# Performance work log

Measured on AMD Instinct MI355X. Metric: run time of the kernel, lower is better.

## Reference

```python
import jax, jax.numpy as jnp
import numpy as np
from math import comb

N_INPUT, N_HIDDEN, N_LATENT = 2, 1024, 16
T, B = 320, 192
DEG = N_LATENT // 2 - 1          # 7
NPTS = DEG + 1                   # 8 control points
LAT = N_LATENT + N_LATENT // 2   # 24

_COMB = jnp.array([comb(DEG, i) for i in range(NPTS)], dtype=jnp.float32)
_I = jnp.arange(NPTS, dtype=jnp.float32)


def setup_inputs() -> dict:
    key = jax.random.key(0)
    ks = jax.random.split(key, 24)
    H = N_HIDDEN
    w = lambda k, shape, sc: (jax.random.normal(k, shape, jnp.float32) * sc)
    return dict(
        x=jax.random.normal(ks[0], (T, B, N_INPUT), jnp.float32),
        latent_ctrlpt=jax.random.normal(ks[1], (B, N_LATENT), jnp.float32),
        latent_ratw=jax.random.uniform(ks[2], (B, N_LATENT // 2), jnp.float32, 0.1, 1.0),
        # h0/c0 projection linears (forward/backward directions)
        W_hf=w(ks[3], (H, LAT), 0.2), b_hf=jnp.zeros((H,), jnp.float32),
        W_hb=w(ks[4], (H, LAT), 0.2), b_hb=jnp.zeros((H,), jnp.float32),
        W_cf=w(ks[5], (H, LAT), 0.2), b_cf=jnp.zeros((H,), jnp.float32),
        W_cb=w(ks[6], (H, LAT), 0.2), b_cb=jnp.zeros((H,), jnp.float32),
        # bi-LSTM weights, PyTorch gate order (i, f, g, o)
        W_ih_f=w(ks[7], (4 * H, N_INPUT), 0.03), W_hh_f=w(ks[8], (4 * H, H), 0.03),
        b_ih_f=jnp.zeros((4 * H,), jnp.float32), b_hh_f=jnp.zeros((4 * H,), jnp.float32),
        W_ih_b=w(ks[9], (4 * H, N_INPUT), 0.03), W_hh_b=w(ks[10], (4 * H, H), 0.03),
        b_ih_b=jnp.zeros((4 * H,), jnp.float32), b_hh_b=jnp.zeros((4 * H,), jnp.float32),
        # t-logits head
        W_log=w(ks[11], (1, 2 * H), 0.03), b_log=jnp.zeros((1,), jnp.float32),
    )


def _lstm_dir(x_tm, h0, c0, W_ih, W_hh, b_ih, b_hh, reverse):
    # x_tm: (T, B, in). Precompute input projection once (compute-efficient).
    xs = jnp.einsum('tbi,gi->tbg', x_tm, W_ih) + b_ih + b_hh  # (T, B, 4H)

    def step(carry, xt):
        h, c = carry
        g = xt + h @ W_hh.T
        i, f, gg, o = jnp.split(g, 4, axis=-1)
        c = jax.nn.sigmoid(f) * c + jax.nn.sigmoid(i) * jnp.tanh(gg)
        h = jax.nn.sigmoid(o) * jnp.tanh(c)
        return (h, c), h

    _, hs = jax.lax.scan(step, (h0, c0), xs, reverse=reverse)
    return hs  # (T, B, H)


def reference(x, latent_ctrlpt, latent_ratw,
              W_hf, b_hf, W_hb, b_hb, W_cf, b_cf, W_cb, b_cb,
              W_ih_f, W_hh_f, b_ih_f, b_hh_f,
              W_ih_b, W_hh_b, b_ih_b, b_hh_b,
              W_log, b_log):
    latent = jnp.concatenate([latent_ctrlpt, latent_ratw], axis=1)  # (B, LAT)
    h0f = jnp.tanh(latent @ W_hf.T + b_hf)
    h0b = jnp.tanh(latent @ W_hb.T + b_hb)
    c0f = jnp.tanh(latent @ W_cf.T + b_cf)
    c0b = jnp.tanh(latent @ W_cb.T + b_cb)

    hf = _lstm_dir(x, h0f, c0f, W_ih_f, W_hh_f, b_ih_f, b_hh_f, reverse=False)
    hb = _lstm_dir(x, h0b, c0b, W_ih_b, W_hh_b, b_ih_b, b_hh_b, reverse=True)
    out = jnp.concatenate([hf, hb], axis=-1)           # (T, B, 2H)
    out = jnp.transpose(out, (1, 0, 2))                # batch_first (B, T, 2H)

    logits = (out @ W_log.T + b_log)[..., 0]           # (B, T)
    ts = jnp.cumsum(jax.nn.softmax(logits, axis=1), axis=1)  # (B, T) in (0, 1]

    P = latent_ctrlpt.reshape(-1, NPTS, 2)             # (B, NPTS, 2)
    r = latent_ratw.reshape(-1, NPTS)                  # (B, NPTS)

    # Rational Bezier curve, batched over B and T (replaces per-sample loop)
    t = ts[..., None]                                   # (B, T, 1)
    basis = _COMB * t ** _I * (1.0 - t) ** (DEG - _I)   # (B, T, NPTS)
    num = basis * r[:, None, :]
    w = num / num.sum(-1, keepdims=True)
    curves = jnp.einsum('btn,bnd->btd', w, P)           # (B, T, 2)

    # mean of squared consecutive control-point distances, averaged over batch
    d2 = ((P[:, 1:, :] - P[:, :-1, :]) ** 2).sum(-1)    # (B, NPTS-1)
    reg = d2.mean()
    return curves, reg
```

## Files before the change

kernel.cpp:

```cpp
#include <hip/hip_runtime.h>
#include <stdint.h>

#define T_STEPS 320
#define BATCH   192
#define HID     1024
#define NBLK    512

typedef unsigned short u16;
typedef __bf16 bf16x8 __attribute__((ext_vector_type(8)));
typedef float  f32x4  __attribute__((ext_vector_type(4)));
typedef unsigned int u32x4 __attribute__((ext_vector_type(4)));

#define OFF_BAR      0u
#define OFF_PART     8192u
#define MEMSET_BYTES 3940352u
#define OFF_C0       3940352u
#define OFF_H        5513216u
#define OFF_WPACK    7086080u
#define OFF_COEF     23863296u
#define WS_NEED      23994368u

#define DMP_WK_STRIDE 3264
#define DMP_BYTES     52224
#define DYN_LDS       52240

__device__ __forceinline__ u16 f2bf(float f) {
  unsigned u = __float_as_uint(f);
  unsigned r = (u + 0x7FFFu + ((u >> 16) & 1u)) >> 16;
  return (u16)r;
}
__device__ __forceinline__ float sigm(float x)   { return 1.f / (1.f + __expf(-x)); }
__device__ __forceinline__ float tanh_f(float x) { return 1.f - 2.f / (1.f + __expf(2.f * x)); }

__global__ void pack_k(const float* __restrict__ Whhf, const float* __restrict__ Whhb,
                       u16* __restrict__ wpack)
{
  int lin = blockIdx.x * 256 + threadIdx.x;
  int lane = lin & 63;
  int cg   = (lin >> 6) & 3;
  int ks   = (lin >> 8) & 31;
  int jsl  = (lin >> 13) & 63;
  int dir  = (lin >> 19) & 1;
  int col  = cg * 16 + (lane & 15);
  int R    = (col & 3) * 1024 + jsl * 16 + (col >> 2);
  int kb   = ks * 32 + (lane >> 4) * 8;
  const float* W = dir ? Whhb : Whhf;
  const float* src = W + (size_t)R * 1024 + kb;
  unsigned w[4];
  #pragma unroll
  for (int e = 0; e < 4; ++e) {
    unsigned lo = f2bf(src[2 * e]);
    unsigned hi = f2bf(src[2 * e + 1]);
    w[e] = lo | (hi << 16);
  }
  *((uint4*)(wpack + (size_t)lin * 8)) = make_uint4(w[0], w[1], w[2], w[3]);
}

__global__ void coef_k(const float* __restrict__ Wihf, const float* __restrict__ bihf,
                       const float* __restrict__ bhhf,
                       const float* __restrict__ Wihb, const float* __restrict__ bihb,
                       const float* __restrict__ bhhb, float* __restrict__ coef)
{
  int id  = blockIdx.x * 256 + threadIdx.x;
  int col = id & 63;
  int jsl = (id >> 6) & 63;
  int dir = (id >> 12) & 1;
  int R   = (col & 3) * 1024 + jsl * 16 + (col >> 2);
  const float* Wih = dir ? Wihb : Wihf;
  const float* bi  = dir ? bihb : bihf;
  const float* bh  = dir ? bhhb : bhhf;
  float4 v;
  v.x = Wih[(size_t)R * 2 + 0];
  v.y = Wih[(size_t)R * 2 + 1];
  v.z = bi[R] + bh[R];
  v.w = 0.f;
  ((float4*)coef)[id] = v;
}

__global__ void init_k(const float* __restrict__ ctrl, const float* __restrict__ ratw,
                       const float* __restrict__ Whf, const float* __restrict__ bhf,
                       const float* __restrict__ Whb, const float* __restrict__ bhb,
                       const float* __restrict__ Wcf, const float* __restrict__ bcf,
                       const float* __restrict__ Wcb, const float* __restrict__ bcb,
                       u16* hb, float* c0)
{
  int idx = blockIdx.x * 256 + threadIdx.x;
  int m = blockIdx.y;
  int b = idx >> 10;
  int h = idx & 1023;
  const float* W  = (m == 0) ? Whf : (m == 1) ? Whb : (m == 2) ? Wcf : Wcb;
  const float* bi = (m == 0) ? bhf : (m == 1) ? bhb : (m == 2) ? bcf : bcb;
  float acc = bi[h];
  const float* wr = W + h * 24;
  #pragma unroll
  for (int k = 0; k < 16; ++k) acc += wr[k] * ctrl[b * 16 + k];
  #pragma unroll
  for (int k = 0; k < 8; ++k)  acc += wr[16 + k] * ratw[b * 8 + k];
  acc = tanh_f(acc);
  if (m < 2) hb[((size_t)(m * 2 + 0) * BATCH + b) * HID + h] = f2bf(acc);
  else       c0[((size_t)(m - 2) * BATCH + b) * HID + h] = acc;
}


#define ALD(S, OB) \
  asm volatile("global_load_dwordx4 %0, %1, off offset:" #OB " sc0 sc1" : "=v"(aq[S][0]) : "v"(ab0)); \
  asm volatile("global_load_dwordx4 %0, %1, off offset:" #OB " sc0 sc1" : "=v"(aq[S][1]) : "v"(ab1)); \
  asm volatile("global_load_dwordx4 %0, %1, off offset:" #OB " sc0 sc1" : "=v"(aq[S][2]) : "v"(ab2));

#define BLD(S, C) { const u16* bp_ = wb + (C) * 2048; \
  asm volatile("global_load_dwordx4 %0, %1, off offset:0"    : "=v"(bq[S][0]) : "v"(bp_)); \
  asm volatile("global_load_dwordx4 %0, %1, off offset:1024" : "=v"(bq[S][1]) : "v"(bp_)); \
  asm volatile("global_load_dwordx4 %0, %1, off offset:2048" : "=v"(bq[S][2]) : "v"(bp_)); \
  asm volatile("global_load_dwordx4 %0, %1, off offset:3072" : "=v"(bq[S][3]) : "v"(bp_)); }

#define SB __builtin_amdgcn_sched_barrier(0);

#define WB(n) \
  asm volatile("s_waitcnt vmcnt(" #n ")" ::: "memory"); \
  __builtin_amdgcn_sched_barrier(0);

#define MM(I) { \
  _Pragma("unroll") \
  for (int mt_ = 0; mt_ < 3; ++mt_) { \
    bf16x8 a_ = __builtin_bit_cast(bf16x8, aq[(I) & 3][mt_]); \
    _Pragma("unroll") \
    for (int n_ = 0; n_ < 4; ++n_) { \
      bf16x8 b_ = __builtin_bit_cast(bf16x8, bq[(I) & 3][n_]); \
      acc[mt_][n_] = __builtin_amdgcn_mfma_f32_16x16x32_bf16(a_, b_, acc[mt_][n_], 0, 0, 0); \
    } \
  } }

#define HST(PT, VL) asm volatile("global_store_short %0, %1, off sc0 sc1" :: "v"(PT), "v"(VL) : "memory")

__launch_bounds__(256, 2)
__global__ void lstm_persist(const float* __restrict__ x,
                             const float* __restrict__ wlog,
                             float* part,
                             const float* __restrict__ c0,
                             u16* hb,
                             const u16* __restrict__ wpack,
                             const float* __restrict__ coef,
                             unsigned* bar)
{
  extern __shared__ char lds[];
  float* DMP = (float*)lds;
  int* ldsflag = (int*)(lds + DMP_BYTES);

  const int tid   = threadIdx.x;
  const int bid   = blockIdx.x;
  const int half  = bid >> 8;
  const int idx   = bid & 255;
  const int grp   = ((idx & 7) + half) & 7;
  const int jsl   = (idx >> 3) + half * 32;
  const int dir   = grp & 1;
  const int bq    = grp >> 1;
  const int wk    = tid >> 6;
  const int lane  = tid & 63;

  if (tid == 0) *ldsflag = 0;

  const int rgrp = tid >> 4;
  const int jj   = tid & 15;
  const int jglob = jsl * 16 + jj;
  float4 cf0, cf1, cf2, cf3;
  {
    const float4* cp = (const float4*)coef + ((dir * 64 + jsl) * 64 + jj * 4);
    cf0 = cp[0]; cf1 = cp[1]; cf2 = cp[2]; cf3 = cp[3];
  }
  const float wlg = wlog[dir * 1024 + jglob];

  float creg[3];
  int   bgm[3];
  #pragma unroll
  for (int mt = 0; mt < 3; ++mt) {
    int r  = rgrp * 3 + mt;
    int bg = bq * 48 + r;
    bgm[mt]  = bg;
    creg[mt] = c0[((size_t)dir * BATCH + bg) * HID + jglob];
  }

  const int arow0 = bq * 48 + 0 * 16 + (lane & 15);
  const int arow1 = arow0 + 16;
  const int arow2 = arow0 + 32;
  const int koff  = wk * 256 + (lane >> 4) * 8;
  const u16* wb   = wpack + (size_t)(dir * 64 + jsl) * 65536
                          + (size_t)wk * 16384 + lane * 8;

  float* pbase = part + ((size_t)(dir * 8 + (jsl & 7)) * BATCH) * T_STEPS;

  unsigned* g1  = bar + (grp << 8) + ((jsl >> 3) << 4);
  unsigned* g2  = bar + (grp << 8) + 128;
  unsigned* rel = bar + (grp << 8) + 144;

  float* dbase = DMP + (size_t)wk * DMP_WK_STRIDE
                     + ((lane >> 4) * 4) * 68 + (lane & 15);
  const int goff = rgrp * 3 * 68 + jj * 4;

  float lpv[3];
  int   lpo[3];

  __syncthreads();

  for (int s = 0; s < T_STEPS; ++s) {
    const int rbuf = s & 1;
    const u16* hsrc = hb + ((size_t)(dir * 2 + rbuf)) * BATCH * HID;
    u16*       hdst = hb + ((size_t)(dir * 2 + (rbuf ^ 1))) * BATCH * HID;
    const u16* ab0 = hsrc + (size_t)arow0 * HID + koff;
    const u16* ab1 = hsrc + (size_t)arow1 * HID + koff;
    const u16* ab2 = hsrc + (size_t)arow2 * HID + koff;

    f32x4 acc[3][4];
    #pragma unroll
    for (int mt = 0; mt < 3; ++mt)
      #pragma unroll
      for (int n = 0; n < 4; ++n)
        acc[mt][n] = (f32x4){0.f, 0.f, 0.f, 0.f};

    u32x4 aq[4][3];
    u32x4 bq[4][4];

    ALD(0, 0)   BLD(0, 0) SB
    ALD(1, 64)  BLD(1, 1) SB
    ALD(2, 128) BLD(2, 2) SB

    ALD(3, 192) BLD(3, 3) WB(21) MM(0)
    ALD(0, 256) BLD(0, 4) WB(21) MM(1)
    ALD(1, 320) BLD(1, 5) WB(21) MM(2)
    ALD(2, 384) BLD(2, 6) WB(21) MM(3)
    ALD(3, 448) BLD(3, 7) WB(21) MM(4)
                          WB(14) MM(5)
                          WB(7)  MM(6)
                          WB(0)  MM(7)

    #pragma unroll
    for (int mt = 0; mt < 3; ++mt)
      #pragma unroll
      for (int n = 0; n < 4; ++n)
        #pragma unroll
        for (int r = 0; r < 4; ++r)
          dbase[(mt * 16 + r) * 68 + n * 16] = acc[mt][n][r];
    __syncthreads();

    const int t_x = dir ? (T_STEPS - 1 - s) : s;

    #pragma unroll
    for (int mt = 0; mt < 3; ++mt) {
      const int ga = goff + mt * 68;
      f32x4 p0 = *(const f32x4*)(DMP + 0 * DMP_WK_STRIDE + ga);
      f32x4 p1 = *(const f32x4*)(DMP + 1 * DMP_WK_STRIDE + ga);
      f32x4 p2 = *(const f32x4*)(DMP + 2 * DMP_WK_STRIDE + ga);
      f32x4 p3 = *(const f32x4*)(DMP + 3 * DMP_WK_STRIDE + ga);
      f32x4 g4 = (p0 + p1) + (p2 + p3);
      int bg = bgm[mt];
      float2 xv = *(const float2*)(x + ((size_t)t_x * BATCH + bg) * 2);
      float pi = g4[0] + cf0.x * xv.x + cf0.y * xv.y + cf0.z;
      float pf = g4[1] + cf1.x * xv.x + cf1.y * xv.y + cf1.z;
      float pg = g4[2] + cf2.x * xv.x + cf2.y * xv.y + cf2.z;
      float po = g4[3] + cf3.x * xv.x + cf3.y * xv.y + cf3.z;
      float ig = sigm(pi), fg = sigm(pf), gv = tanh_f(pg), og = sigm(po);
      float c = fg * creg[mt] + ig * gv;
      creg[mt] = c;
      float h = og * tanh_f(c);
      u16* hp = hdst + (size_t)bg * HID + jglob;
      unsigned hv = (unsigned)f2bf(h);
      HST(hp, hv);
      float lp = h * wlg;
      lp += __shfl_xor(lp, 1);
      lp += __shfl_xor(lp, 2);
      lp += __shfl_xor(lp, 4);
      lp += __shfl_xor(lp, 8);
      lpv[mt] = lp;
      lpo[mt] = bg * T_STEPS + t_x;
    }

    asm volatile("s_waitcnt vmcnt(0)" ::: "memory");
    __syncthreads();

    if (jj == 0) {
      atomicAdd(&pbase[lpo[0]], lpv[0]);
      atomicAdd(&pbase[lpo[1]], lpv[1]);
      atomicAdd(&pbase[lpo[2]], lpv[2]);
    }

    if (tid == 0) {
      bool last = false;
      unsigned o1 = __hip_atomic_fetch_add(g1, 1u, __ATOMIC_RELAXED, __HIP_MEMORY_SCOPE_AGENT);
      if (o1 == (unsigned)(s * 8 + 7)) {
        unsigned o2 = __hip_atomic_fetch_add(g2, 1u, __ATOMIC_RELAXED, __HIP_MEMORY_SCOPE_AGENT);
        if (o2 == (unsigned)(s * 8 + 7)) {
          unsigned rv = (unsigned)(s + 1);
          asm volatile("global_store_dword %0, %1, off sc0 sc1" :: "v"(rel), "v"(rv) : "memory");
          last = true;
        }
      }
      if (!last) {
        long guard = 0;
        unsigned rv;
        for (;;) {
          asm volatile("global_load_dword %0, %1, off sc0 sc1" : "=v"(rv) : "v"(rel));
          asm volatile("s_waitcnt vmcnt(0)" ::: "memory");
          if ((int)rv >= s + 1) break;
          if (++guard > (1L << 20)) { *ldsflag = 1; break; }
          __builtin_amdgcn_s_sleep(2);
        }
      }
    }
    __syncthreads();
    if (*ldsflag) return;
  }
}

__global__ void post_k(const float* __restrict__ part, const float* __restrict__ ctrl,
                       const float* __restrict__ ratw, float* __restrict__ out)
{
  __shared__ float sh[T_STEPS + 64];
  const int b = blockIdx.x;
  const int t = threadIdx.x;
  float l = 0.f;
  #pragma unroll
  for (int p = 0; p < 16; ++p)
    l += part[((size_t)p * BATCH + b) * T_STEPS + t];
  sh[t] = l;
  __syncthreads();
  if (t < 64) {
    float mm = sh[t];
    for (int i = t + 64; i < T_STEPS; i += 64) mm = fmaxf(mm, sh[i]);
    #pragma unroll
    for (int o = 32; o; o >>= 1) mm = fmaxf(mm, __shfl_xor(mm, o));
    if (t == 0) sh[T_STEPS] = mm;
  }
  __syncthreads();
  const float m = sh[T_STEPS];
  float e = __expf(l - m);
  __syncthreads();
  sh[t] = e;
  __syncthreads();
  for (int off = 1; off < T_STEPS; off <<= 1) {
    float v = (t >= off) ? sh[t - off] : 0.f;
    __syncthreads();
    sh[t] += v;
    __syncthreads();
  }
  const float total = sh[T_STEPS - 1];
  const float ts = sh[t] / total;

  float px[8], py[8], rr[8];
  #pragma unroll
  for (int n = 0; n < 8; ++n) {
    px[n] = ctrl[b * 16 + 2 * n];
    py[n] = ctrl[b * 16 + 2 * n + 1];
    rr[n] = ratw[b * 8 + n];
  }
  const float C[8] = {1.f, 7.f, 21.f, 35.f, 35.f, 21.f, 7.f, 1.f};
  float tp[8], up[8];
  tp[0] = 1.f; up[0] = 1.f;
  const float u = 1.f - ts;
  #pragma unroll
  for (int n = 1; n < 8; ++n) { tp[n] = tp[n - 1] * ts; up[n] = up[n - 1] * u; }
  float den = 0.f, nx = 0.f, ny = 0.f;
  #pragma unroll
  for (int n = 0; n < 8; ++n) {
    float w = C[n] * tp[n] * up[7 - n] * rr[n];
    den += w; nx += w * px[n]; ny += w * py[n];
  }
  out[(b * T_STEPS + t) * 2 + 0] = nx / den;
  out[(b * T_STEPS + t) * 2 + 1] = ny / den;

  if (b == 0) {
    __syncthreads();
    if (t < BATCH) {
      float s2 = 0.f;
      #pragma unroll
      for (int n = 0; n < 7; ++n) {
        float dx = ctrl[t * 16 + 2 * n + 2] - ctrl[t * 16 + 2 * n + 0];
        float dy = ctrl[t * 16 + 2 * n + 3] - ctrl[t * 16 + 2 * n + 1];
        s2 += dx * dx + dy * dy;
      }
      sh[t] = s2;
    }
    __syncthreads();
    if (t == 0) {
      float tot = 0.f;
      for (int i = 0; i < BATCH; ++i) tot += sh[i];
      out[BATCH * T_STEPS * 2] = tot / (float)(BATCH * 7);
    }
  }
}

extern "C" void kernel_launch(void* const* d_in, const int* in_sizes, int n_in,
                              void* d_out, int out_size, void* d_ws, size_t ws_size,
                              hipStream_t stream)
{
  const float* x    = (const float*)d_in[0];
  const float* ctrl = (const float*)d_in[1];
  const float* ratw = (const float*)d_in[2];
  const float* Whf  = (const float*)d_in[3];
  const float* bhf  = (const float*)d_in[4];
  const float* Whb  = (const float*)d_in[5];
  const float* bhb  = (const float*)d_in[6];
  const float* Wcf  = (const float*)d_in[7];
  const float* bcf  = (const float*)d_in[8];
  const float* Wcb  = (const float*)d_in[9];
  const float* bcb  = (const float*)d_in[10];
  const float* Wihf = (const float*)d_in[11];
  const float* Whhf = (const float*)d_in[12];
  const float* bihf = (const float*)d_in[13];
  const float* bhhf = (const float*)d_in[14];
  const float* Wihb = (const float*)d_in[15];
  const float* Whhb = (const float*)d_in[16];
  const float* bihb = (const float*)d_in[17];
  const float* bhhb = (const float*)d_in[18];
  const float* Wlog = (const float*)d_in[19];
  float* out = (float*)d_out;
  char*  ws  = (char*)d_ws;
  if (ws_size < (size_t)WS_NEED) return;

  unsigned* bar    = (unsigned*)(ws + OFF_BAR);
  float*    part   = (float*)(ws + OFF_PART);
  float*    c0     = (float*)(ws + OFF_C0);
  u16*      hb     = (u16*)(ws + OFF_H);
  u16*      wpack  = (u16*)(ws + OFF_WPACK);
  float*    coef   = (float*)(ws + OFF_COEF);

  hipMemsetAsync(ws, 0, MEMSET_BYTES, stream);
  pack_k<<<4096, 256, 0, stream>>>(Whhf, Whhb, wpack);
  coef_k<<<32, 256, 0, stream>>>(Wihf, bihf, bhhf, Wihb, bihb, bhhb, coef);
  init_k<<<dim3(768, 4), 256, 0, stream>>>(ctrl, ratw, Whf, bhf, Whb, bhb,
                                           Wcf, bcf, Wcb, bcb, hb, c0);
  hipFuncSetAttribute((const void*)lstm_persist,
                      hipFuncAttributeMaxDynamicSharedMemorySize, DYN_LDS);
  lstm_persist<<<NBLK, 256, DYN_LDS, stream>>>(x, Wlog, part, c0, hb, wpack, coef, bar);
  post_k<<<BATCH, T_STEPS, 0, stream>>>(part, ctrl, ratw, out);
}
```

Before: 4.224 ms.

## Replace two-level barrier with flat counter polling and remap block-to-group assignment

Replaces the hierarchical arrive/release barrier, where the last arriver stores a release flag, with a flat scheme. Each block increments its sub-group counter, then 8 lanes of wave 0 poll all 8 counters and sum them through shuffles until the total reaches 64 per step. Blocks are also remapped so that direction and batch quarter come from the low bits of the block index. The aim is to remove the serial second atomic and the release store from the critical path of each step, in exchange for more polling traffic on the shared counters.

```diff
diff --git a/kernel.cpp b/kernel.cpp
--- a/kernel.cpp
+++ b/kernel.cpp
@@ -150,12 +150,13 @@
   const int bid   = blockIdx.x;
   const int half  = bid >> 8;
   const int idx   = bid & 255;
-  const int grp   = ((idx & 7) + half) & 7;
-  const int jsl   = (idx >> 3) + half * 32;
-  const int dir   = grp & 1;
-  const int bq    = grp >> 1;
+  const int dir   = idx & 1;
+  const int jsl   = idx >> 2;
+  const int bquad = half * 2 + ((idx >> 1) & 1);
+  const int grp   = dir * 4 + bquad;
   const int wk    = tid >> 6;
   const int lane  = tid & 63;
+  const int wave  = tid >> 6;
 
   if (tid == 0) *ldsflag = 0;
 
@@ -174,12 +175,12 @@
   #pragma unroll
   for (int mt = 0; mt < 3; ++mt) {
     int r  = rgrp * 3 + mt;
-    int bg = bq * 48 + r;
+    int bg = bquad * 48 + r;
     bgm[mt]  = bg;
     creg[mt] = c0[((size_t)dir * BATCH + bg) * HID + jglob];
   }
 
-  const int arow0 = bq * 48 + 0 * 16 + (lane & 15);
+  const int arow0 = bquad * 48 + 0 * 16 + (lane & 15);
   const int arow1 = arow0 + 16;
   const int arow2 = arow0 + 32;
   const int koff  = wk * 256 + (lane >> 4) * 8;
@@ -188,9 +189,8 @@
 
   float* pbase = part + ((size_t)(dir * 8 + (jsl & 7)) * BATCH) * T_STEPS;
 
-  unsigned* g1  = bar + (grp << 8) + ((jsl >> 3) << 4);
-  unsigned* g2  = bar + (grp << 8) + 128;
-  unsigned* rel = bar + (grp << 8) + 144;
+  unsigned* g1 = bar + (grp << 8) + ((jsl >> 3) << 4);
+  const unsigned* cpoll = bar + (grp << 8) + ((lane & 7) << 4);
 
   float* dbase = DMP + (size_t)wk * DMP_WK_STRIDE
                      + ((lane >> 4) * 4) * 68 + (lane & 15);
@@ -282,27 +282,24 @@
       atomicAdd(&pbase[lpo[2]], lpv[2]);
     }
 
-    if (tid == 0) {
-      bool last = false;
-      unsigned o1 = __hip_atomic_fetch_add(g1, 1u, __ATOMIC_RELAXED, __HIP_MEMORY_SCOPE_AGENT);
-      if (o1 == (unsigned)(s * 8 + 7)) {
-        unsigned o2 = __hip_atomic_fetch_add(g2, 1u, __ATOMIC_RELAXED, __HIP_MEMORY_SCOPE_AGENT);
-        if (o2 == (unsigned)(s * 8 + 7)) {
-          unsigned rv = (unsigned)(s + 1);
-          asm volatile("global_store_dword %0, %1, off sc0 sc1" :: "v"(rel), "v"(rv) : "memory");
-          last = true;
+    if (wave == 0) {
+      if (lane == 0)
+        __hip_atomic_fetch_add(g1, 1u, __ATOMIC_RELAXED, __HIP_MEMORY_SCOPE_AGENT);
+      const unsigned target = (unsigned)(s + 1) * 64u;
+      long guard = 0;
+      for (;;) {
+        unsigned cv = 0;
+        if (lane < 8) {
+          asm volatile("global_load_dword %0, %1, off sc0 sc1" : "=v"(cv) : "v"(cpoll));
+          asm volatile("s_waitcnt vmcnt(0)" ::: "memory");
         }
-      }
-      if (!last) {
-        long guard = 0;
-        unsigned rv;
-        for (;;) {
-          asm volatile("global_load_dword %0, %1, off sc0 sc1" : "=v"(rv) : "v"(rel));
-          asm volatile("s_waitcnt vmcnt(0)" ::: "memory");
-          if ((int)rv >= s + 1) break;
-          if (++guard > (1L << 20)) { *ldsflag = 1; break; }
-          __builtin_amdgcn_s_sleep(2);
-        }
+        cv += __shfl_xor(cv, 1);
+        cv += __shfl_xor(cv, 2);
+        cv += __shfl_xor(cv, 4);
+        cv = __shfl(cv, 0);
+        if (cv >= target) break;
+        if (++guard > (1L << 18)) { if (lane == 0) *ldsflag = 1; break; }
+        __builtin_amdgcn_s_sleep(1);
       }
     }
     __syncthreads();
```

After: 4.596 ms. 1.09x slower.
